# Optimization experiments

Measured on AMD Instinct MI355X. Metric: run time of the kernel, lower is better.

## Reference

```python
import jax, jax.numpy as jnp
import numpy as np

EPS = 1e-5

def conv3d(x, w, b):
    y = jax.lax.conv_general_dilated(x, w, (1, 1, 1), [(1, 1), (1, 1), (1, 1)],
                                     dimension_numbers=('NCDHW', 'OIDHW', 'NCDHW'))
    return y + b[None, :, None, None, None]

def batchnorm(x, g, b):
    # training-mode BN: biased batch statistics over (N, D, H, W)
    m = jnp.mean(x, axis=(0, 2, 3, 4), keepdims=True)
    v = jnp.mean((x - m) ** 2, axis=(0, 2, 3, 4), keepdims=True)
    return (x - m) * jax.lax.rsqrt(v + EPS) * g[None, :, None, None, None] + b[None, :, None, None, None]

def deform_conv3d(x, offset, w, b):
    # x: (B,C,D,H,W); offset: (B, 3*27, D,H,W); w: (O,C,3,3,3)
    B, C, D, H, W = x.shape
    N = 27
    xp = jnp.pad(x, ((0, 0), (0, 0), (1, 1), (1, 1), (1, 1)))
    Dp, Hp, Wp = D + 2, H + 2, W + 2
    off = offset.reshape(B, 3, N, D, H, W)
    kk = jnp.arange(3, dtype=x.dtype) - 1.0  # kernel taps -1,0,1
    kd, kh, kw = [a.reshape(-1) for a in jnp.meshgrid(kk, kk, kk, indexing='ij')]
    # sampling positions in padded coords: p0 (=out idx + pad) + kernel tap + learned offset
    pd = jnp.clip((jnp.arange(D, dtype=x.dtype) + 1.0)[None, None, :, None, None]
                  + kd[None, :, None, None, None] + off[:, 0], 0.0, Dp - 1)
    ph = jnp.clip((jnp.arange(H, dtype=x.dtype) + 1.0)[None, None, None, :, None]
                  + kh[None, :, None, None, None] + off[:, 1], 0.0, Hp - 1)
    pw = jnp.clip((jnp.arange(W, dtype=x.dtype) + 1.0)[None, None, None, None, :]
                  + kw[None, :, None, None, None] + off[:, 2], 0.0, Wp - 1)
    q0d = jnp.clip(jnp.floor(pd), 0, Dp - 2); td = jnp.clip(pd - q0d, 0.0, 1.0)
    q0h = jnp.clip(jnp.floor(ph), 0, Hp - 2); th = jnp.clip(ph - q0h, 0.0, 1.0)
    q0w = jnp.clip(jnp.floor(pw), 0, Wp - 2); tw = jnp.clip(pw - q0w, 0.0, 1.0)
    q0d = q0d.astype(jnp.int32); q0h = q0h.astype(jnp.int32); q0w = q0w.astype(jnp.int32)
    xf = xp.reshape(B, C, -1)
    acc = jnp.zeros((B, C, N, D, H, W), dtype=x.dtype)
    for i in (0, 1):
        for j in (0, 1):
            for k in (0, 1):
                idx = ((q0d + i) * Hp + (q0h + j)) * Wp + (q0w + k)  # (B,N,D,H,W)
                g = ((td if i else 1.0 - td) * (th if j else 1.0 - th) * (tw if k else 1.0 - tw))
                gath = jnp.take_along_axis(xf, idx.reshape(B, 1, -1), axis=2).reshape(B, C, N, D, H, W)
                acc = acc + g[:, None] * gath
    out = jnp.einsum('bcndhw,ocn->bodhw', acc, w.reshape(w.shape[0], C, N))
    return out + b[None, :, None, None, None]


def setup_inputs() -> dict:
    ks = jax.random.split(jax.random.key(0), 16)
    s = 0.05
    f32 = jnp.float32
    return {
        'x': jax.random.normal(ks[0], (4, 1, 28, 28, 8), f32),
        'c1w': jax.random.normal(ks[1], (32, 1, 3, 3, 3), f32) * s, 'c1b': jnp.zeros((32,), f32),
        'g1': jnp.ones((32,), f32), 'b1': jnp.zeros((32,), f32),
        'c2w': jax.random.normal(ks[2], (64, 32, 3, 3, 3), f32) * s, 'c2b': jnp.zeros((64,), f32),
        'g2': jnp.ones((64,), f32), 'b2': jnp.zeros((64,), f32),
        'c3w': jax.random.normal(ks[3], (128, 64, 3, 3, 3), f32) * s, 'c3b': jnp.zeros((128,), f32),
        'g3': jnp.ones((128,), f32), 'b3': jnp.zeros((128,), f32),
        'ow': jax.random.normal(ks[4], (81, 128, 3, 3, 3), f32) * s, 'ob': jnp.zeros((81,), f32),
        'dw': jax.random.normal(ks[5], (128, 128, 3, 3, 3), f32) * s, 'db': jnp.zeros((128,), f32),
        'g4': jnp.ones((128,), f32), 'b4': jnp.zeros((128,), f32),
        'fcw': jax.random.normal(ks[6], (10, 128), f32) * s, 'fcb': jnp.zeros((10,), f32),
    }


def reference(x, c1w, c1b, g1, b1, c2w, c2b, g2, b2, c3w, c3b, g3, b3,
              ow, ob, dw, db, g4, b4, fcw, fcb):
    h = batchnorm(jax.nn.relu(conv3d(x, c1w, c1b)), g1, b1)
    h = batchnorm(jax.nn.relu(conv3d(h, c2w, c2b)), g2, b2)
    h = batchnorm(jax.nn.relu(conv3d(h, c3w, c3b)), g3, b3)
    offsets = conv3d(h, ow, ob)
    h = batchnorm(jax.nn.relu(deform_conv3d(h, offsets, dw, db)), g4, b4)
    pooled = jnp.mean(h, axis=(2, 3, 4))  # avg_pool over full (28,28,d) extent
    logits = pooled @ fcw.T + fcb
    return jax.nn.log_softmax(logits, axis=1), offsets
```

## Files before the change

### kernel.cpp

```cpp
#include <hip/hip_runtime.h>
#include <hip/hip_bf16.h>
#include <math.h>

#define BB 4
#define SP 6272
#define NSP 25088
#define EPS 1e-5f

typedef unsigned short u16;
typedef __attribute__((ext_vector_type(8))) short v8s;
typedef __attribute__((ext_vector_type(4))) float v4f;

__device__ __forceinline__ u16 f2b(float f) {
    unsigned u = __float_as_uint(f);
    return (u16)((u + 0x7fffu + ((u >> 16) & 1u)) >> 16);
}
__device__ __forceinline__ float b2f(u16 s) {
    return __uint_as_float(((unsigned)s) << 16);
}
__device__ __forceinline__ float b2f_lo(unsigned x) { return __uint_as_float(x << 16); }
__device__ __forceinline__ float b2f_hi(unsigned x) { return __uint_as_float(x & 0xffff0000u); }
__device__ __forceinline__ unsigned pk2(float a, float b) {
    __hip_bfloat162 h = __float22bfloat162_rn(make_float2(a, b));
    unsigned u;
    __builtin_memcpy(&u, &h, 4);
    return u;
}

__global__ __launch_bounds__(256) __attribute__((amdgpu_waves_per_eu(1, 4)))
void conv1_shfl(const float* __restrict__ X, const float* __restrict__ Wt,
                const float* __restrict__ bias, u16* __restrict__ Ybf,
                float* __restrict__ s_sum, float* __restrict__ s_sq)
{
    const int OT = 16;
    __shared__ float red[4][32];
    int xblk = blockIdx.x;
    int sblk = (xblk & 7) * 13 + (xblk >> 3);
    if (sblk >= 98) return;
    int t = threadIdx.x;
    int s = sblk * 256 + t;
    int b = s / SP;
    int sp = s - b * SP;
    int d = sp / 224;
    int r = sp - d * 224;
    int h = r >> 3;
    int w = r & 7;
    int o0 = blockIdx.y * OT;

    float mdh[9]; int odh[9];
    #pragma unroll
    for (int i = 0; i < 3; i++) {
        int dd = d + i - 1;
        float md = ((unsigned)dd < 28u) ? 1.f : 0.f;
        int ddc = min(max(dd, 0), 27);
        #pragma unroll
        for (int j = 0; j < 3; j++) {
            int hh = h + j - 1;
            float mh = ((unsigned)hh < 28u) ? 1.f : 0.f;
            int hhc = min(max(hh, 0), 27);
            mdh[i * 3 + j] = md * mh;
            odh[i * 3 + j] = ddc * 224 + hhc * 8 + w;
        }
    }
    float mw0 = (w > 0) ? 1.f : 0.f;
    float mw2 = (w < 7) ? 1.f : 0.f;

    float acc[OT];
    #pragma unroll
    for (int oo = 0; oo < OT; oo++) acc[oo] = bias[o0 + oo];

    const float* xc = X + (size_t)b * SP;
    #pragma unroll
    for (int t9 = 0; t9 < 9; t9++) {
        float x0 = xc[odh[t9]];
        float m = mdh[t9];
        float xm = __shfl_up(x0, 1, 64) * (m * mw0);
        float xz = x0 * m;
        float xp = __shfl_down(x0, 1, 64) * (m * mw2);
        #pragma unroll
        for (int oo = 0; oo < OT; oo++) {
            const float* wp = Wt + (size_t)(o0 + oo) * 27 + t9 * 3;
            acc[oo] = fmaf(xm, wp[0], acc[oo]);
            acc[oo] = fmaf(xz, wp[1], acc[oo]);
            acc[oo] = fmaf(xp, wp[2], acc[oo]);
        }
    }
    float sv[OT];
    #pragma unroll
    for (int oo = 0; oo < OT; oo++) sv[oo] = fmaxf(acc[oo], 0.f);

    unsigned pk[8];
    #pragma unroll
    for (int j = 0; j < 8; j++) pk[j] = pk2(sv[2 * j], sv[2 * j + 1]);
    u16* row = Ybf + (size_t)(b * SP + sp) * 32 + o0;
    *(uint4*)(row)     = make_uint4(pk[0], pk[1], pk[2], pk[3]);
    *(uint4*)(row + 8) = make_uint4(pk[4], pk[5], pk[6], pk[7]);

    int l = t & 63, wvv = t >> 6;
    #pragma unroll
    for (int oo = 0; oo < OT; oo++) {
        float ss = sv[oo], qv = ss * ss;
        #pragma unroll
        for (int m = 1; m < 64; m <<= 1) {
            ss += __shfl_xor(ss, m, 64);
            qv += __shfl_xor(qv, m, 64);
        }
        if (l == 0) { red[wvv][oo] = ss; red[wvv][16 + oo] = qv; }
    }
    __syncthreads();
    if (t < 32) {
        float tot = red[0][t] + red[1][t] + red[2][t] + red[3][t];
        if (t < 16) atomicAdd(&s_sum[o0 + t], tot);
        else        atomicAdd(&s_sq[o0 + t - 16], tot);
    }
}

__global__ __launch_bounds__(256) void prepack_all(const float* __restrict__ c2w,
        const float* __restrict__ c3w, const float* __restrict__ ow,
        const float* __restrict__ dw, u16* __restrict__ wpk2,
        u16* __restrict__ wpk3, u16* __restrict__ wpko, u16* __restrict__ dwa,
        float* __restrict__ ws0)
{
    int bx = blockIdx.x;
    if (bx >= 4536) {
        int i = (bx - 4536) * 256 + threadIdx.x;
        if (i < 2048) ws0[i] = 0.f;
        return;
    }
    int idx = bx * 256 + threadIdx.x;
    if (idx < 55296) {
        int i = idx;
        int j = i & 7, r = (i >> 3) & 15, q = (i >> 7) & 3;
        int ot = (i >> 9) & 3, t = i >> 11;
        int o = ot * 16 + r, c = q * 8 + j;
        wpk2[i] = f2b(c2w[((size_t)o * 32 + c) * 27 + t]);
    } else if (idx < 276480) {
        int i = idx - 55296;
        int j = i & 7, r = (i >> 3) & 15, q = (i >> 7) & 3;
        int ch = (i >> 9) & 1, ot = (i >> 10) & 7, t = i >> 13;
        int o = ot * 16 + r, c = ch * 32 + q * 8 + j;
        wpk3[i] = f2b(c3w[((size_t)o * 64 + c) * 27 + t]);
    } else if (idx < 718848) {
        int i = idx - 276480;
        int j = i & 7, r = (i >> 3) & 15, q = (i >> 7) & 3;
        int ch = (i >> 9) & 3, ot = (i >> 11) & 7, t = i >> 14;
        int o = ot * 16 + r, c = ch * 32 + q * 8 + j;
        wpko[i] = f2b((o < 81) ? ow[((size_t)o * 128 + c) * 27 + t] : 0.f);
    } else {
        int i = idx - 718848;
        int j = i & 7, r = (i >> 3) & 15, q = (i >> 7) & 3;
        int kc = (i >> 9) & 3, ot = (i >> 11) & 7, n = i >> 14;
        int o = ot * 16 + r, c = kc * 32 + q * 8 + j;
        dwa[i] = f2b(dw[((size_t)o * 128 + c) * 27 + n]);
    }
}

template<int CIN, int OPAD, bool OFFOUT, bool BNIN, bool WIDE>
__global__ __launch_bounds__(256) __attribute__((amdgpu_waves_per_eu(1, 4)))
void conv_mfma(const u16* __restrict__ X, const u16* __restrict__ Wpk,
               const float* __restrict__ bias, u16* __restrict__ Ybf,
               float* __restrict__ offs, float* __restrict__ s_sum,
               float* __restrict__ s_sq, const float* __restrict__ in_sum,
               const float* __restrict__ in_sq, const float* __restrict__ in_g,
               const float* __restrict__ in_b)
{
    const int HS = CIN + 8;
    const int NOT = OPAD / 16;
    const int NC = CIN / 32;
    __shared__ u16 xs[160 * HS];
    __shared__ float scin[BNIN ? CIN : 1], shin[BNIN ? CIN : 1];

    int tid = threadIdx.x;
    int fid = blockIdx.x;
    int g = (fid & 7) * 98 + (fid >> 3);
    int b = g / 196;
    int rem = g - b * 196;
    int d0 = (rem / 14) * 2, h0 = (rem % 14) * 2;

    if (BNIN) {
        if (tid < CIN) {
            float m = in_sum[tid] * (1.f / NSP);
            float v = in_sq[tid] * (1.f / NSP) - m * m;
            float sc = in_g[tid] * rsqrtf(v + EPS);
            scin[tid] = sc;
            shin[tid] = in_b[tid] - m * sc;
        }
        __syncthreads();
    }

    const int NCH = CIN / 8;
    for (int idx = tid; idx < 160 * NCH; idx += 256) {
        int pos = idx / NCH, ch = idx - pos * NCH;
        int dz = pos / 40, r2 = pos - dz * 40;
        int hz = r2 / 10, wz = r2 - hz * 10;
        int dd = d0 + dz - 1, hh = h0 + hz - 1, ww = wz - 1;
        uint4 val = make_uint4(0, 0, 0, 0);
        if ((unsigned)dd < 28u && (unsigned)hh < 28u && (unsigned)ww < 8u) {
            val = *(const uint4*)(X + ((size_t)(b * SP + dd * 224 + hh * 8 + ww) * CIN + ch * 8));
            if (BNIN) {
                int cb = ch * 8;
                float f0 = b2f_lo(val.x) * scin[cb]     + shin[cb];
                float f1 = b2f_hi(val.x) * scin[cb + 1] + shin[cb + 1];
                float f2 = b2f_lo(val.y) * scin[cb + 2] + shin[cb + 2];
                float f3 = b2f_hi(val.y) * scin[cb + 3] + shin[cb + 3];
                float f4 = b2f_lo(val.z) * scin[cb + 4] + shin[cb + 4];
                float f5 = b2f_hi(val.z) * scin[cb + 5] + shin[cb + 5];
                float f6 = b2f_lo(val.w) * scin[cb + 6] + shin[cb + 6];
                float f7 = b2f_hi(val.w) * scin[cb + 7] + shin[cb + 7];
                val.x = pk2(f0, f1); val.y = pk2(f2, f3);
                val.z = pk2(f4, f5); val.w = pk2(f6, f7);
            }
        }
        *(uint4*)(xs + pos * HS + ch * 8) = val;
    }
    __syncthreads();

    int l = tid & 63, wv = tid >> 6;
    int q = l >> 4, r = l & 15;
    int hl = r >> 3, wl = r & 7;

    if (OFFOUT) {
        int dl = wv >> 1;
        int ot0 = (wv & 1) * 3;
        const u16* ap = xs + ((4 + hl + 1) * 10 + wl + 1) * HS + 8 * q + dl * 40 * HS;
        v4f acc[3];
        acc[0] = (v4f){0.f,0.f,0.f,0.f};
        acc[1] = (v4f){0.f,0.f,0.f,0.f};
        acc[2] = (v4f){0.f,0.f,0.f,0.f};
        #pragma unroll
        for (int t = 0; t < 27; t++) {
            const int koff = ((t / 9) - 1) * 40 + (((t / 3) % 3) - 1) * 10 + (t % 3) - 1;
            const u16* wt = Wpk + ((size_t)(t * NOT + ot0) * NC << 9) + l * 8;
            #pragma unroll
            for (int ch = 0; ch < NC; ch++) {
                v8s a0 = *(const v8s*)(ap + koff * HS + ch * 32);
                v8s b0 = *(const v8s*)(wt + ch * 512);
                v8s b1 = *(const v8s*)(wt + (NC + ch) * 512);
                v8s b2 = *(const v8s*)(wt + (2 * NC + ch) * 512);
                acc[0] = __builtin_amdgcn_mfma_f32_16x16x32_bf16(a0, b0, acc[0], 0, 0, 0);
                acc[1] = __builtin_amdgcn_mfma_f32_16x16x32_bf16(a0, b1, acc[1], 0, 0, 0);
                acc[2] = __builtin_amdgcn_mfma_f32_16x16x32_bf16(a0, b2, acc[2], 0, 0, 0);
            }
        }
        int o0 = ot0 * 16 + r;
        #pragma unroll
        for (int j = 0; j < 3; j++) {
            int o = o0 + 16 * j;
            if (o < 81) {
                float bo = bias[o];
                #pragma unroll
                for (int rg = 0; rg < 4; rg++) {
                    int rowl = q * 4 + rg;
                    int sp = (d0 + dl) * 224 + (h0 + (rowl >> 3)) * 8 + (rowl & 7);
                    offs[((size_t)(b * 81 + o)) * SP + sp] = acc[j][rg] + bo;
                }
            }
        }
        return;
    }

    const u16* a0p = xs + ((4 + hl + 1) * 10 + wl + 1) * HS + 8 * q;
    const u16* a1p = a0p + 40 * HS;

    if (WIDE) {
        v4f acc[2][2];
        acc[0][0] = (v4f){0.f,0.f,0.f,0.f}; acc[0][1] = (v4f){0.f,0.f,0.f,0.f};
        acc[1][0] = (v4f){0.f,0.f,0.f,0.f}; acc[1][1] = (v4f){0.f,0.f,0.f,0.f};
        #pragma unroll
        for (int t = 0; t < 27; t++) {
            const int koff = ((t / 9) - 1) * 40 + (((t / 3) % 3) - 1) * 10 + (t % 3) - 1;
            const u16* wt  = Wpk + ((size_t)(t * NOT + wv) * NC << 9) + l * 8;
            const u16* wt2 = wt + (size_t)4 * NC * 512;
            #pragma unroll
            for (int ch = 0; ch < NC; ch++) {
                v8s a0 = *(const v8s*)(a0p + koff * HS + ch * 32);
                v8s a1 = *(const v8s*)(a1p + koff * HS + ch * 32);
                v8s b0 = *(const v8s*)(wt + ch * 512);
                v8s b1 = *(const v8s*)(wt2 + ch * 512);
                acc[0][0] = __builtin_amdgcn_mfma_f32_16x16x32_bf16(a0, b0, acc[0][0], 0, 0, 0);
                acc[0][1] = __builtin_amdgcn_mfma_f32_16x16x32_bf16(a1, b0, acc[0][1], 0, 0, 0);
                acc[1][0] = __builtin_amdgcn_mfma_f32_16x16x32_bf16(a0, b1, acc[1][0], 0, 0, 0);
                acc[1][1] = __builtin_amdgcn_mfma_f32_16x16x32_bf16(a1, b1, acc[1][1], 0, 0, 0);
            }
        }
        #pragma unroll
        for (int oti = 0; oti < 2; oti++) {
            int o_base = wv * 16 + oti * 64;
            int oo = o_base + r;
            float bo = bias[oo];
            float rs = 0.f, rq = 0.f;
            #pragma unroll
            for (int s2 = 0; s2 < 2; s2++) {
                v4f A = acc[oti][s2];
                #pragma unroll
                for (int rg = 0; rg < 4; rg++) {
                    int rowl = q * 4 + rg;
                    int sp = (d0 + s2) * 224 + (h0 + (rowl >> 3)) * 8 + (rowl & 7);
                    float v = fmaxf(A[rg] + bo, 0.f);
                    Ybf[(size_t)(b * SP + sp) * OPAD + oo] = f2b(v);
                    rs += v; rq += v * v;
                }
            }
            rs += __shfl_xor(rs, 16, 64); rs += __shfl_xor(rs, 32, 64);
            rq += __shfl_xor(rq, 16, 64); rq += __shfl_xor(rq, 32, 64);
            if (l < 16) { atomicAdd(&s_sum[o_base + l], rs); atomicAdd(&s_sq[o_base + l], rq); }
        }
        return;
    }

    int o_base = blockIdx.y * 64 + wv * 16;
    int o = o_base + r;
    int otg = o_base >> 4;

    v4f acc0 = {0.f, 0.f, 0.f, 0.f}, acc1 = {0.f, 0.f, 0.f, 0.f};
    #pragma unroll
    for (int t = 0; t < 27; t++) {
        const int koff = ((t / 9) - 1) * 40 + (((t / 3) % 3) - 1) * 10 + (t % 3) - 1;
        const u16* wt = Wpk + ((size_t)(t * NOT + otg) * NC << 9) + l * 8;
        #pragma unroll
        for (int ch = 0; ch < NC; ch++) {
            v8s a0 = *(const v8s*)(a0p + koff * HS + ch * 32);
            v8s a1 = *(const v8s*)(a1p + koff * HS + ch * 32);
            v8s bf = *(const v8s*)(wt + ch * 512);
            acc0 = __builtin_amdgcn_mfma_f32_16x16x32_bf16(a0, bf, acc0, 0, 0, 0);
            acc1 = __builtin_amdgcn_mfma_f32_16x16x32_bf16(a1, bf, acc1, 0, 0, 0);
        }
    }

    {
        float bo = bias[o];
        float rs = 0.f, rq = 0.f;
        #pragma unroll
        for (int s2 = 0; s2 < 2; s2++) {
            v4f A = s2 ? acc1 : acc0;
            #pragma unroll
            for (int rg = 0; rg < 4; rg++) {
                int rowl = q * 4 + rg;
                int sp = (d0 + s2) * 224 + (h0 + (rowl >> 3)) * 8 + (rowl & 7);
                float v = fmaxf(A[rg] + bo, 0.f);
                Ybf[(size_t)(b * SP + sp) * OPAD + o] = f2b(v);
                rs += v; rq += v * v;
            }
        }
        rs += __shfl_xor(rs, 16, 64); rs += __shfl_xor(rs, 32, 64);
        rq += __shfl_xor(rq, 16, 64); rq += __shfl_xor(rq, 32, 64);
        if (l < 16) { atomicAdd(&s_sum[o_base + l], rs); atomicAdd(&s_sq[o_base + l], rq); }
    }
}

template<int C>
__global__ __launch_bounds__(256) void bn_bf(const u16* __restrict__ Y,
        const float* __restrict__ s_sum, const float* __restrict__ s_sq,
        const float* __restrict__ g, const float* __restrict__ bb,
        u16* __restrict__ Xo)
{
    __shared__ float sc_s[C], sh_s[C];
    int t = threadIdx.x;
    if (t < C) {
        float m  = s_sum[t] * (1.f / NSP);
        float v  = s_sq[t] * (1.f / NSP) - m * m;
        float sc = g[t] * rsqrtf(v + EPS);
        sc_s[t] = sc;
        sh_s[t] = bb[t] - m * sc;
    }
    __syncthreads();
    int idx = blockIdx.x * 256 + t;
    uint4 v = ((const uint4*)Y)[idx];
    int cb = (idx & (C / 8 - 1)) * 8;
    float f0 = b2f_lo(v.x) * sc_s[cb]     + sh_s[cb];
    float f1 = b2f_hi(v.x) * sc_s[cb + 1] + sh_s[cb + 1];
    float f2 = b2f_lo(v.y) * sc_s[cb + 2] + sh_s[cb + 2];
    float f3 = b2f_hi(v.y) * sc_s[cb + 3] + sh_s[cb + 3];
    float f4 = b2f_lo(v.z) * sc_s[cb + 4] + sh_s[cb + 4];
    float f5 = b2f_hi(v.z) * sc_s[cb + 5] + sh_s[cb + 5];
    float f6 = b2f_lo(v.w) * sc_s[cb + 6] + sh_s[cb + 6];
    float f7 = b2f_hi(v.w) * sc_s[cb + 7] + sh_s[cb + 7];
    uint4 pk;
    pk.x = pk2(f0, f1); pk.y = pk2(f2, f3);
    pk.z = pk2(f4, f5); pk.w = pk2(f6, f7);
    ((uint4*)Xo)[idx] = pk;
}

__global__ __launch_bounds__(256) __attribute__((amdgpu_waves_per_eu(1, 4)))
void deform_pool(const u16* __restrict__ Ht, const float* __restrict__ OFF,
                 const u16* __restrict__ Wa, const float* __restrict__ db,
                 float* __restrict__ pooledraw, float* __restrict__ sumsq4)
{
    __shared__ float offs_lds[81 * 32];
    __shared__ int ig_s[32][8][2];
    __shared__ u16 Vb[32][136];
    __shared__ float reds[128], redq[128];

    int fid = blockIdx.x;
    int xcd = fid & 7;
    int local = fid >> 3;
    if (local >= 98) return;
    int b = xcd >> 1;
    int d = (xcd & 1) * 14 + local / 7;
    int h0 = (local % 7) * 4;

    int t = threadIdx.x;
    if (t < 128) { reds[t] = 0.f; redq[t] = 0.f; }

    int gp = t >> 3, gcr = t & 7;
    int glh = gp >> 3, gw = gp & 7, gh = h0 + glh;
    int co = t & 15, pg = t >> 4;
    int l = t & 63, wv = t >> 6;
    int q = l >> 4, r = l & 15;

    v4f acc[2][2];
    acc[0][0] = (v4f){0.f,0.f,0.f,0.f}; acc[0][1] = (v4f){0.f,0.f,0.f,0.f};
    acc[1][0] = (v4f){0.f,0.f,0.f,0.f}; acc[1][1] = (v4f){0.f,0.f,0.f,0.f};

    const u16* hb = Ht + (size_t)b * SP * 128;

    for (int i = t; i < 2592; i += 256) {
        int ch = i >> 5, p = i & 31;
        offs_lds[i] = OFF[(size_t)b * 81 * SP + (size_t)ch * SP
                          + d * 224 + (h0 + (p >> 3)) * 8 + (p & 7)];
    }

    for (int n = 0; n < 27; n++) {
        __syncthreads();
        {
            int kd = n / 9 - 1, kh = (n / 3) % 3 - 1, kw = n % 3 - 1;
            float od  = offs_lds[n * 32 + gp];
            float oh  = offs_lds[(27 + n) * 32 + gp];
            float owv = offs_lds[(54 + n) * 32 + gp];
            float pd = fminf(fmaxf((float)(d + 1 + kd) + od, 0.f), 29.f);
            float ph = fminf(fmaxf((float)(gh + 1 + kh) + oh, 0.f), 29.f);
            float pw = fminf(fmaxf((float)(gw + 1 + kw) + owv, 0.f), 9.f);
            float qd = fminf(floorf(pd), 28.f);
            float qh = fminf(floorf(ph), 28.f);
            float qw = fminf(floorf(pw), 8.f);
            float td = fminf(pd - qd, 1.f);
            float th = fminf(ph - qh, 1.f);
            float tw = fminf(pw - qw, 1.f);
            int iqd = (int)qd - 1, iqh = (int)qh - 1, iqw = (int)qw - 1;
            int i = gcr >> 2, j = (gcr >> 1) & 1, k = gcr & 1;
            int du = iqd + i, hu = iqh + j, wu = iqw + k;
            bool val = (unsigned)du < 28u && (unsigned)hu < 28u && (unsigned)wu < 8u;
            float gg = (i ? td : 1.f - td) * (j ? th : 1.f - th) * (k ? tw : 1.f - tw);
            ig_s[gp][gcr][0] = val ? (du * 224 + hu * 8 + wu) : 0;
            ig_s[gp][gcr][1] = __float_as_int(val ? gg : 0.f);
        }
        __syncthreads();
        #pragma unroll
        for (int pp = 0; pp < 2; pp++) {
            int p = pg * 2 + pp;
            float va[8] = {0.f,0.f,0.f,0.f,0.f,0.f,0.f,0.f};
            #pragma unroll
            for (int cr = 0; cr < 8; cr++) {
                int2 pr = *(const int2*)&ig_s[p][cr][0];
                float gg = __int_as_float(pr.y);
                uint4 xv = *(const uint4*)(hb + (size_t)pr.x * 128 + co * 8);
                va[0] = fmaf(gg, b2f_lo(xv.x), va[0]);
                va[1] = fmaf(gg, b2f_hi(xv.x), va[1]);
                va[2] = fmaf(gg, b2f_lo(xv.y), va[2]);
                va[3] = fmaf(gg, b2f_hi(xv.y), va[3]);
                va[4] = fmaf(gg, b2f_lo(xv.z), va[4]);
                va[5] = fmaf(gg, b2f_hi(xv.z), va[5]);
                va[6] = fmaf(gg, b2f_lo(xv.w), va[6]);
                va[7] = fmaf(gg, b2f_hi(xv.w), va[7]);
            }
            uint4 pk;
            pk.x = pk2(va[0], va[1]); pk.y = pk2(va[2], va[3]);
            pk.z = pk2(va[4], va[5]); pk.w = pk2(va[6], va[7]);
            *(uint4*)&Vb[p][co * 8] = pk;
        }
        __syncthreads();
        const u16* wn = Wa + (size_t)n * 16384;
        #pragma unroll
        for (int oti = 0; oti < 2; oti++) {
            int ot = wv * 2 + oti;
            #pragma unroll
            for (int kc = 0; kc < 4; kc++) {
                v8s af = *(const v8s*)(wn + ((((ot * 4 + kc) * 4 + q) * 16 + r) * 8));
                v8s bf0 = *(const v8s*)&Vb[r][kc * 32 + q * 8];
                v8s bf1 = *(const v8s*)&Vb[16 + r][kc * 32 + q * 8];
                acc[oti][0] = __builtin_amdgcn_mfma_f32_16x16x32_bf16(af, bf0, acc[oti][0], 0, 0, 0);
                acc[oti][1] = __builtin_amdgcn_mfma_f32_16x16x32_bf16(af, bf1, acc[oti][1], 0, 0, 0);
            }
        }
    }

    #pragma unroll
    for (int oti = 0; oti < 2; oti++) {
        #pragma unroll
        for (int rg = 0; rg < 4; rg++) {
            int o = (wv * 2 + oti) * 16 + q * 4 + rg;
            float bo = db[o];
            float v0 = fmaxf(acc[oti][0][rg] + bo, 0.f);
            float v1 = fmaxf(acc[oti][1][rg] + bo, 0.f);
            float s = v0 + v1, qq = v0 * v0 + v1 * v1;
            s += __shfl_xor(s, 1, 64);  qq += __shfl_xor(qq, 1, 64);
            s += __shfl_xor(s, 2, 64);  qq += __shfl_xor(qq, 2, 64);
            s += __shfl_xor(s, 4, 64);  qq += __shfl_xor(qq, 4, 64);
            s += __shfl_xor(s, 8, 64);  qq += __shfl_xor(qq, 8, 64);
            if (r == 0) { atomicAdd(&reds[o], s); atomicAdd(&redq[o], qq); }
        }
    }
    __syncthreads();
    if (t < 128) {
        atomicAdd(&pooledraw[b * 128 + t], reds[t]);
        atomicAdd(&sumsq4[t], redq[t]);
    }
}

__global__ __launch_bounds__(256) void final_head_emit(const float* __restrict__ pooledraw,
        const float* __restrict__ sumsq4, const float* __restrict__ g4,
        const float* __restrict__ b4, const float* __restrict__ fcw,
        const float* __restrict__ fcb, float* __restrict__ out)
{
    int t = threadIdx.x;
    __shared__ float pooled_s[4][128];
    __shared__ float logits[4][10];
    if (t < 128) {
        float s0 = pooledraw[t], s1 = pooledraw[128 + t];
        float s2 = pooledraw[256 + t], s3 = pooledraw[384 + t];
        float tot = s0 + s1 + s2 + s3;
        float m  = tot * (1.f / NSP);
        float v  = sumsq4[t] * (1.f / NSP) - m * m;
        float sc = g4[t] * rsqrtf(v + EPS);
        float sh = b4[t] - m * sc;
        pooled_s[0][t] = s0 * (1.f / SP) * sc + sh;
        pooled_s[1][t] = s1 * (1.f / SP) * sc + sh;
        pooled_s[2][t] = s2 * (1.f / SP) * sc + sh;
        pooled_s[3][t] = s3 * (1.f / SP) * sc + sh;
    }
    __syncthreads();
    if (t < 40) {
        int b = t / 10, j = t % 10;
        float l = fcb[j];
        for (int c = 0; c < 128; c++) l = fmaf(pooled_s[b][c], fcw[j * 128 + c], l);
        logits[b][j] = l;
    }
    __syncthreads();
    if (t < 4) {
        float mx = -1e30f;
        for (int j = 0; j < 10; j++) mx = fmaxf(mx, logits[t][j]);
        float se = 0.f;
        for (int j = 0; j < 10; j++) se += expf(logits[t][j] - mx);
        float lse = mx + logf(se);
        for (int j = 0; j < 10; j++) out[t * 10 + j] = logits[t][j] - lse;
    }
}

extern "C" void kernel_launch(void* const* d_in, const int* in_sizes, int n_in,
                              void* d_out, int out_size, void* d_ws, size_t ws_size,
                              hipStream_t stream)
{
    (void)in_sizes; (void)n_in; (void)out_size; (void)ws_size;
    const float* x   = (const float*)d_in[0];
    const float* c1w = (const float*)d_in[1];
    const float* c1b = (const float*)d_in[2];
    const float* g1  = (const float*)d_in[3];
    const float* b1  = (const float*)d_in[4];
    const float* c2w = (const float*)d_in[5];
    const float* c2b = (const float*)d_in[6];
    const float* g2  = (const float*)d_in[7];
    const float* b2  = (const float*)d_in[8];
    const float* c3w = (const float*)d_in[9];
    const float* c3b = (const float*)d_in[10];
    const float* g3  = (const float*)d_in[11];
    const float* b3  = (const float*)d_in[12];
    const float* ow  = (const float*)d_in[13];
    const float* ob  = (const float*)d_in[14];
    const float* dw  = (const float*)d_in[15];
    const float* db  = (const float*)d_in[16];
    const float* g4  = (const float*)d_in[17];
    const float* b4  = (const float*)d_in[18];
    const float* fcw = (const float*)d_in[19];
    const float* fcb = (const float*)d_in[20];

    float* ws = (float*)d_ws;
    float* S1 = ws + 0,   *Q1 = ws + 32;
    float* S2 = ws + 64,  *Q2 = ws + 128;
    float* S3 = ws + 192, *Q3 = ws + 320;
    float* PO = ws + 448;
    float* Q4 = ws + 960;
    u16* y1bf = (u16*)(ws + 2048);
    u16* y2bf = y1bf + 802816;
    u16* y3bf = y2bf + 1605632;
    u16* x3bf = y3bf + 3211264;
    u16* wpk2 = x3bf + 3211264;
    u16* wpk3 = wpk2 + 55296;
    u16* wpko = wpk3 + 221184;
    u16* dwa  = wpko + 442368;

    float* outf = (float*)d_out;
    float* offp = outf + 40;

    prepack_all<<<4544, 256, 0, stream>>>(c2w, c3w, ow, dw, wpk2, wpk3, wpko, dwa, ws);

    conv1_shfl<<<dim3(104, 2), 256, 0, stream>>>(x, c1w, c1b, y1bf, S1, Q1);

    conv_mfma<32, 64, false, true, false><<<dim3(784, 1), 256, 0, stream>>>(
        y1bf, wpk2, c2b, y2bf, nullptr, S2, Q2, S1, Q1, g1, b1);

    conv_mfma<64, 128, false, true, true><<<dim3(784, 1), 256, 0, stream>>>(
        y2bf, wpk3, c3b, y3bf, nullptr, S3, Q3, S2, Q2, g2, b2);

    bn_bf<128><<<1568, 256, 0, stream>>>(y3bf, S3, Q3, g3, b3, x3bf);

    conv_mfma<128, 128, true, false, false><<<dim3(784, 1), 256, 0, stream>>>(
        x3bf, wpko, ob, nullptr, offp, nullptr, nullptr, nullptr, nullptr, nullptr, nullptr);

    deform_pool<<<800, 256, 0, stream>>>(x3bf, offp, dwa, db, PO, Q4);
    final_head_emit<<<1, 256, 0, stream>>>(PO, Q4, g4, b4, fcw, fcb, outf);
}
```

Measured before the change: 340.6 us.

## Fuse conv1 into prepack, split deform taps across blocks, fold BN into offset conv

Conv1 now runs as extra blocks inside the prepack launch. It writes per-block partial statistics instead of atomics, and conv2 reduces those partials itself. The offset conv applies BN3 on input, and bn_bf runs in place afterwards, which removes the x3bf buffer. deform_pool splits its 27 taps over twice as many blocks, combined through atomic partial sums and a last-arriver counter. This adds parallelism and one fewer launch, at the cost of extra global atomics, a partial buffer that must be zeroed, and relying on an untested fence/counter ordering.

New measurement: 671.2 us. +97.1%, slower.

```diff
diff --git a/kernel.cpp b/kernel.cpp
--- a/kernel.cpp
+++ b/kernel.cpp
@@ -27,107 +27,116 @@
     return u;
 }
 
-__global__ __launch_bounds__(256) __attribute__((amdgpu_waves_per_eu(1, 4)))
-void conv1_shfl(const float* __restrict__ X, const float* __restrict__ Wt,
-                const float* __restrict__ bias, u16* __restrict__ Ybf,
-                float* __restrict__ s_sum, float* __restrict__ s_sq)
-{
-    const int OT = 16;
-    __shared__ float red[4][32];
-    int xblk = blockIdx.x;
-    int sblk = (xblk & 7) * 13 + (xblk >> 3);
-    if (sblk >= 98) return;
-    int t = threadIdx.x;
-    int s = sblk * 256 + t;
-    int b = s / SP;
-    int sp = s - b * SP;
-    int d = sp / 224;
-    int r = sp - d * 224;
-    int h = r >> 3;
-    int w = r & 7;
-    int o0 = blockIdx.y * OT;
-
-    float mdh[9]; int odh[9];
-    #pragma unroll
-    for (int i = 0; i < 3; i++) {
-        int dd = d + i - 1;
-        float md = ((unsigned)dd < 28u) ? 1.f : 0.f;
-        int ddc = min(max(dd, 0), 27);
-        #pragma unroll
-        for (int j = 0; j < 3; j++) {
-            int hh = h + j - 1;
-            float mh = ((unsigned)hh < 28u) ? 1.f : 0.f;
-            int hhc = min(max(hh, 0), 27);
-            mdh[i * 3 + j] = md * mh;
-            odh[i * 3 + j] = ddc * 224 + hhc * 8 + w;
-        }
-    }
-    float mw0 = (w > 0) ? 1.f : 0.f;
-    float mw2 = (w < 7) ? 1.f : 0.f;
-
-    float acc[OT];
-    #pragma unroll
-    for (int oo = 0; oo < OT; oo++) acc[oo] = bias[o0 + oo];
-
-    const float* xc = X + (size_t)b * SP;
-    #pragma unroll
-    for (int t9 = 0; t9 < 9; t9++) {
-        float x0 = xc[odh[t9]];
-        float m = mdh[t9];
-        float xm = __shfl_up(x0, 1, 64) * (m * mw0);
-        float xz = x0 * m;
-        float xp = __shfl_down(x0, 1, 64) * (m * mw2);
-        #pragma unroll
-        for (int oo = 0; oo < OT; oo++) {
-            const float* wp = Wt + (size_t)(o0 + oo) * 27 + t9 * 3;
-            acc[oo] = fmaf(xm, wp[0], acc[oo]);
-            acc[oo] = fmaf(xz, wp[1], acc[oo]);
-            acc[oo] = fmaf(xp, wp[2], acc[oo]);
-        }
-    }
-    float sv[OT];
-    #pragma unroll
-    for (int oo = 0; oo < OT; oo++) sv[oo] = fmaxf(acc[oo], 0.f);
-
-    unsigned pk[8];
-    #pragma unroll
-    for (int j = 0; j < 8; j++) pk[j] = pk2(sv[2 * j], sv[2 * j + 1]);
-    u16* row = Ybf + (size_t)(b * SP + sp) * 32 + o0;
-    *(uint4*)(row)     = make_uint4(pk[0], pk[1], pk[2], pk[3]);
-    *(uint4*)(row + 8) = make_uint4(pk[4], pk[5], pk[6], pk[7]);
-
-    int l = t & 63, wvv = t >> 6;
-    #pragma unroll
-    for (int oo = 0; oo < OT; oo++) {
-        float ss = sv[oo], qv = ss * ss;
-        #pragma unroll
-        for (int m = 1; m < 64; m <<= 1) {
-            ss += __shfl_xor(ss, m, 64);
-            qv += __shfl_xor(qv, m, 64);
-        }
-        if (l == 0) { red[wvv][oo] = ss; red[wvv][16 + oo] = qv; }
-    }
-    __syncthreads();
-    if (t < 32) {
-        float tot = red[0][t] + red[1][t] + red[2][t] + red[3][t];
-        if (t < 16) atomicAdd(&s_sum[o0 + t], tot);
-        else        atomicAdd(&s_sq[o0 + t - 16], tot);
-    }
-}
-
 __global__ __launch_bounds__(256) void prepack_all(const float* __restrict__ c2w,
         const float* __restrict__ c3w, const float* __restrict__ ow,
         const float* __restrict__ dw, u16* __restrict__ wpk2,
         u16* __restrict__ wpk3, u16* __restrict__ wpko, u16* __restrict__ dwa,
-        float* __restrict__ ws0)
+        float* __restrict__ ws0, float* __restrict__ PP,
+        const float* __restrict__ X, const float* __restrict__ Wt,
+        const float* __restrict__ c1b, u16* __restrict__ Ybf,
+        float* __restrict__ P1s, float* __restrict__ P1q)
 {
     int bx = blockIdx.x;
+    int tid = threadIdx.x;
+
+    if (bx >= 7680) {
+        const int OT = 16;
+        __shared__ float red[4][32];
+        int c = bx - 7680;
+        int xblk = c % 104;
+        int o0 = (c / 104) * OT;
+        int sblk = (xblk & 7) * 13 + (xblk >> 3);
+        if (sblk >= 98) return;
+        int t = tid;
+        int s = sblk * 256 + t;
+        int b = s / SP;
+        int sp = s - b * SP;
+        int d = sp / 224;
+        int r = sp - d * 224;
+        int h = r >> 3;
+        int w = r & 7;
+
+        float mdh[9]; int odh[9];
+        #pragma unroll
+        for (int i = 0; i < 3; i++) {
+            int dd = d + i - 1;
+            float md = ((unsigned)dd < 28u) ? 1.f : 0.f;
+            int ddc = min(max(dd, 0), 27);
+            #pragma unroll
+            for (int j = 0; j < 3; j++) {
+                int hh = h + j - 1;
+                float mh = ((unsigned)hh < 28u) ? 1.f : 0.f;
+                int hhc = min(max(hh, 0), 27);
+                mdh[i * 3 + j] = md * mh;
+                odh[i * 3 + j] = ddc * 224 + hhc * 8 + w;
+            }
+        }
+        float mw0 = (w > 0) ? 1.f : 0.f;
+        float mw2 = (w < 7) ? 1.f : 0.f;
+
+        float acc[OT];
+        #pragma unroll
+        for (int oo = 0; oo < OT; oo++) acc[oo] = c1b[o0 + oo];
+
+        const float* xc = X + (size_t)b * SP;
+        #pragma unroll
+        for (int t9 = 0; t9 < 9; t9++) {
+            float x0 = xc[odh[t9]];
+            float m = mdh[t9];
+            float xm = __shfl_up(x0, 1, 64) * (m * mw0);
+            float xz = x0 * m;
+            float xp = __shfl_down(x0, 1, 64) * (m * mw2);
+            #pragma unroll
+            for (int oo = 0; oo < OT; oo++) {
+                const float* wp = Wt + (size_t)(o0 + oo) * 27 + t9 * 3;
+                acc[oo] = fmaf(xm, wp[0], acc[oo]);
+                acc[oo] = fmaf(xz, wp[1], acc[oo]);
+                acc[oo] = fmaf(xp, wp[2], acc[oo]);
+            }
+        }
+        float sv[OT];
+        #pragma unroll
+        for (int oo = 0; oo < OT; oo++) sv[oo] = fmaxf(acc[oo], 0.f);
+
+        unsigned pk[8];
+        #pragma unroll
+        for (int j = 0; j < 8; j++) pk[j] = pk2(sv[2 * j], sv[2 * j + 1]);
+        u16* row = Ybf + (size_t)(b * SP + sp) * 32 + o0;
+        *(uint4*)(row)     = make_uint4(pk[0], pk[1], pk[2], pk[3]);
+        *(uint4*)(row + 8) = make_uint4(pk[4], pk[5], pk[6], pk[7]);
+
+        int l = t & 63, wvv = t >> 6;
+        #pragma unroll
+        for (int oo = 0; oo < OT; oo++) {
+            float ss = sv[oo], qv = ss * ss;
+            #pragma unroll
+            for (int m = 1; m < 64; m <<= 1) {
+                ss += __shfl_xor(ss, m, 64);
+                qv += __shfl_xor(qv, m, 64);
+            }
+            if (l == 0) { red[wvv][oo] = ss; red[wvv][16 + oo] = qv; }
+        }
+        __syncthreads();
+        if (t < 32) {
+            float tot = red[0][t] + red[1][t] + red[2][t] + red[3][t];
+            if (t < 16) P1s[sblk * 32 + o0 + t] = tot;
+            else        P1q[sblk * 32 + o0 + (t - 16)] = tot;
+        }
+        return;
+    }
+
+    if (bx >= 4544) {
+        int i = (bx - 4544) * 256 + tid;
+        ((uint4*)PP)[i] = make_uint4(0, 0, 0, 0);
+        return;
+    }
+
     if (bx >= 4536) {
-        int i = (bx - 4536) * 256 + threadIdx.x;
+        int i = (bx - 4536) * 256 + tid;
         if (i < 2048) ws0[i] = 0.f;
         return;
     }
-    int idx = bx * 256 + threadIdx.x;
+    int idx = bx * 256 + tid;
     if (idx < 55296) {
         int i = idx;
         int j = i & 7, r = (i >> 3) & 15, q = (i >> 7) & 3;
@@ -155,7 +164,7 @@
     }
 }
 
-template<int CIN, int OPAD, bool OFFOUT, bool BNIN, bool WIDE>
+template<int CIN, int OPAD, bool OFFOUT, bool BNIN, bool WIDE, bool PARTIN>
 __global__ __launch_bounds__(256) __attribute__((amdgpu_waves_per_eu(1, 4)))
 void conv_mfma(const u16* __restrict__ X, const u16* __restrict__ Wpk,
                const float* __restrict__ bias, u16* __restrict__ Ybf,
@@ -178,14 +187,37 @@
     int d0 = (rem / 14) * 2, h0 = (rem % 14) * 2;
 
     if (BNIN) {
-        if (tid < CIN) {
-            float m = in_sum[tid] * (1.f / NSP);
-            float v = in_sq[tid] * (1.f / NSP) - m * m;
-            float sc = in_g[tid] * rsqrtf(v + EPS);
-            scin[tid] = sc;
-            shin[tid] = in_b[tid] - m * sc;
-        }
-        __syncthreads();
+        if (PARTIN) {
+            __shared__ float ps[8][32], pq[8][32];
+            int ch = tid & 31, ck = tid >> 5;
+            float s = 0.f, qq = 0.f;
+            for (int k = ck; k < 98; k += 8) {
+                s  += in_sum[k * 32 + ch];
+                qq += in_sq[k * 32 + ch];
+            }
+            ps[ck][ch] = s; pq[ck][ch] = qq;
+            __syncthreads();
+            if (tid < CIN) {
+                float m = 0.f, vq = 0.f;
+                #pragma unroll
+                for (int k2 = 0; k2 < 8; k2++) { m += ps[k2][tid]; vq += pq[k2][tid]; }
+                m *= (1.f / NSP);
+                vq = vq * (1.f / NSP) - m * m;
+                float sc = in_g[tid] * rsqrtf(vq + EPS);
+                scin[tid] = sc;
+                shin[tid] = in_b[tid] - m * sc;
+            }
+            __syncthreads();
+        } else {
+            if (tid < CIN) {
+                float m = in_sum[tid] * (1.f / NSP);
+                float v = in_sq[tid] * (1.f / NSP) - m * m;
+                float sc = in_g[tid] * rsqrtf(v + EPS);
+                scin[tid] = sc;
+                shin[tid] = in_b[tid] - m * sc;
+            }
+            __syncthreads();
+        }
     }
 
     const int NCH = CIN / 8;
@@ -384,17 +416,22 @@
 __global__ __launch_bounds__(256) __attribute__((amdgpu_waves_per_eu(1, 4)))
 void deform_pool(const u16* __restrict__ Ht, const float* __restrict__ OFF,
                  const u16* __restrict__ Wa, const float* __restrict__ db,
-                 float* __restrict__ pooledraw, float* __restrict__ sumsq4)
+                 float* __restrict__ pooledraw, float* __restrict__ sumsq4,
+                 float* __restrict__ PP, unsigned* __restrict__ cnt)
 {
     __shared__ float offs_lds[81 * 32];
     __shared__ int ig_s[32][8][2];
     __shared__ u16 Vb[32][136];
     __shared__ float reds[128], redq[128];
-
-    int fid = blockIdx.x;
+    __shared__ unsigned done_s;
+
+    int bid = blockIdx.x;
+    int half = bid >= 800;
+    int fid = half ? bid - 800 : bid;
     int xcd = fid & 7;
     int local = fid >> 3;
     if (local >= 98) return;
+    int dense = xcd * 98 + local;
     int b = xcd >> 1;
     int d = (xcd & 1) * 14 + local / 7;
     int h0 = (local % 7) * 4;
@@ -420,7 +457,9 @@
                           + d * 224 + (h0 + (p >> 3)) * 8 + (p & 7)];
     }
 
-    for (int n = 0; n < 27; n++) {
+    int n_lo = half ? 14 : 0;
+    int n_hi = half ? 27 : 14;
+    for (int n = n_lo; n < n_hi; n++) {
         __syncthreads();
         {
             int kd = n / 9 - 1, kh = (n / 3) % 3 - 1, kw = n % 3 - 1;
@@ -484,14 +523,40 @@
         }
     }
 
+    float* pp = PP + (size_t)dense * 4096 + t * 16;
+    #pragma unroll
+    for (int oti = 0; oti < 2; oti++)
+        #pragma unroll
+        for (int pt = 0; pt < 2; pt++)
+            #pragma unroll
+            for (int rg = 0; rg < 4; rg++)
+                atomicAdd(&pp[(oti * 2 + pt) * 4 + rg], acc[oti][pt][rg]);
+    __syncthreads();
+    if (t == 0) {
+        __threadfence();
+        done_s = atomicAdd(&cnt[dense], 1u);
+    }
+    __syncthreads();
+    if (done_s != 1u) return;
+
+    __threadfence();
+    float4 t00 = *(const float4*)(pp + 0);
+    float4 t01 = *(const float4*)(pp + 4);
+    float4 t10 = *(const float4*)(pp + 8);
+    float4 t11 = *(const float4*)(pp + 12);
+    float tt[2][2][4] = {
+        {{t00.x, t00.y, t00.z, t00.w}, {t01.x, t01.y, t01.z, t01.w}},
+        {{t10.x, t10.y, t10.z, t10.w}, {t11.x, t11.y, t11.z, t11.w}}
+    };
+
     #pragma unroll
     for (int oti = 0; oti < 2; oti++) {
         #pragma unroll
         for (int rg = 0; rg < 4; rg++) {
             int o = (wv * 2 + oti) * 16 + q * 4 + rg;
             float bo = db[o];
-            float v0 = fmaxf(acc[oti][0][rg] + bo, 0.f);
-            float v1 = fmaxf(acc[oti][1][rg] + bo, 0.f);
+            float v0 = fmaxf(tt[oti][0][rg] + bo, 0.f);
+            float v1 = fmaxf(tt[oti][1][rg] + bo, 0.f);
             float s = v0 + v1, qq = v0 * v0 + v1 * v1;
             s += __shfl_xor(s, 1, 64);  qq += __shfl_xor(qq, 1, 64);
             s += __shfl_xor(s, 2, 64);  qq += __shfl_xor(qq, 2, 64);
@@ -574,38 +639,40 @@
     const float* fcb = (const float*)d_in[20];
 
     float* ws = (float*)d_ws;
-    float* S1 = ws + 0,   *Q1 = ws + 32;
     float* S2 = ws + 64,  *Q2 = ws + 128;
     float* S3 = ws + 192, *Q3 = ws + 320;
     float* PO = ws + 448;
     float* Q4 = ws + 960;
-    u16* y1bf = (u16*)(ws + 2048);
+    unsigned* cnt = (unsigned*)(ws + 1152);
+    float* P1s = ws + 4096;
+    float* P1q = ws + 7232;
+    u16* y1bf = (u16*)(ws + 16384);
     u16* y2bf = y1bf + 802816;
     u16* y3bf = y2bf + 1605632;
-    u16* x3bf = y3bf + 3211264;
-    u16* wpk2 = x3bf + 3211264;
+    u16* wpk2 = y3bf + 3211264;
     u16* wpk3 = wpk2 + 55296;
     u16* wpko = wpk3 + 221184;
     u16* dwa  = wpko + 442368;
+    float* PP = (float*)(dwa + 442368);
 
     float* outf = (float*)d_out;
     float* offp = outf + 40;
 
-    prepack_all<<<4544, 256, 0, stream>>>(c2w, c3w, ow, dw, wpk2, wpk3, wpko, dwa, ws);
-
-    conv1_shfl<<<dim3(104, 2), 256, 0, stream>>>(x, c1w, c1b, y1bf, S1, Q1);
-
-    conv_mfma<32, 64, false, true, false><<<dim3(784, 1), 256, 0, stream>>>(
-        y1bf, wpk2, c2b, y2bf, nullptr, S2, Q2, S1, Q1, g1, b1);
-
-    conv_mfma<64, 128, false, true, true><<<dim3(784, 1), 256, 0, stream>>>(
+    prepack_all<<<7888, 256, 0, stream>>>(c2w, c3w, ow, dw, wpk2, wpk3, wpko, dwa,
+                                          ws, PP, x, c1w, c1b, y1bf, P1s, P1q);
+
+    conv_mfma<32, 64, false, true, false, true><<<784, 256, 0, stream>>>(
+        y1bf, wpk2, c2b, y2bf, nullptr, S2, Q2, P1s, P1q, g1, b1);
+
+    conv_mfma<64, 128, false, true, true, false><<<784, 256, 0, stream>>>(
         y2bf, wpk3, c3b, y3bf, nullptr, S3, Q3, S2, Q2, g2, b2);
 
-    bn_bf<128><<<1568, 256, 0, stream>>>(y3bf, S3, Q3, g3, b3, x3bf);
-
-    conv_mfma<128, 128, true, false, false><<<dim3(784, 1), 256, 0, stream>>>(
-        x3bf, wpko, ob, nullptr, offp, nullptr, nullptr, nullptr, nullptr, nullptr, nullptr);
-
-    deform_pool<<<800, 256, 0, stream>>>(x3bf, offp, dwa, db, PO, Q4);
+    conv_mfma<128, 128, true, true, false, false><<<784, 256, 0, stream>>>(
+        y3bf, wpko, ob, nullptr, offp, nullptr, nullptr, S3, Q3, g3, b3);
+
+    bn_bf<128><<<1568, 256, 0, stream>>>(y3bf, S3, Q3, g3, b3, y3bf);
+
+    deform_pool<<<1600, 256, 0, stream>>>(y3bf, offp, dwa, db, PO, Q4, PP, cnt);
+
     final_head_emit<<<1, 256, 0, stream>>>(PO, Q4, g4, b4, fcw, fcb, outf);
 }
```
